# Performance work log

Hardware: AMD Instinct MI355X
Metric: run time of the kernel (lower is better)

The kernel has to match this reference:

```python
import jax, jax.numpy as jnp
import numpy as np

B, T, F, H = 256, 512, 64, 128


def _uniform(key, shape, stdv):
    return jax.random.uniform(key, shape, jnp.float32, -stdv, stdv)


def setup_inputs() -> dict:
    key = jax.random.key(0)
    ks = jax.random.split(key, 24)
    values = jax.random.normal(ks[0], (B, T, F), jnp.float32)
    masks = (jax.random.uniform(ks[1], (B, T, F)) < 0.8).astype(jnp.float32)
    deltas = jax.random.uniform(ks[2], (B, T, F), jnp.float32)
    labels = (jax.random.uniform(ks[3], (B, 1)) < 0.5).astype(jnp.float32)
    is_train = (jax.random.uniform(ks[4], (B, 1)) < 0.8).astype(jnp.float32)
    sH = 1.0 / np.sqrt(H)
    sF = 1.0 / np.sqrt(F)
    # temp_decay_h: Linear F -> H (stdv = 1/sqrt(out) per reset_parameters)
    W_dh = _uniform(ks[5], (H, F), sH); b_dh = _uniform(ks[6], (H,), sH)
    # temp_decay_x: diag F -> F
    W_dx = _uniform(ks[7], (F, F), sF); b_dx = _uniform(ks[8], (F,), sF)
    # hist_reg: Linear H -> F (torch Linear stdv = 1/sqrt(in))
    W_hr = _uniform(ks[9], (F, H), sH); b_hr = _uniform(ks[10], (F,), sH)
    # feat_reg: F -> F with zeroed diagonal mask
    W_fr = _uniform(ks[11], (F, F), sF); b_fr = _uniform(ks[12], (F,), sF)
    # weight_combine: Linear 2F -> F
    s2F = 1.0 / np.sqrt(2 * F)
    W_wc = _uniform(ks[13], (F, 2 * F), s2F); b_wc = _uniform(ks[14], (F,), s2F)
    # LSTMCell(2F, H): torch init uniform(-1/sqrt(H), 1/sqrt(H)), gate order i,f,g,o
    W_ih = _uniform(ks[15], (4 * H, 2 * F), sH); b_ih = _uniform(ks[16], (4 * H,), sH)
    W_hh = _uniform(ks[17], (4 * H, H), sH); b_hh = _uniform(ks[18], (4 * H,), sH)
    # out: Linear H -> 1
    W_out = _uniform(ks[19], (1, H), sH); b_out = _uniform(ks[20], (1,), sH)
    return dict(values=values, masks=masks, deltas=deltas, labels=labels, is_train=is_train,
                W_dh=W_dh, b_dh=b_dh, W_dx=W_dx, b_dx=b_dx, W_hr=W_hr, b_hr=b_hr,
                W_fr=W_fr, b_fr=b_fr, W_wc=W_wc, b_wc=b_wc,
                W_ih=W_ih, b_ih=b_ih, W_hh=W_hh, b_hh=b_hh, W_out=W_out, b_out=b_out)


def _forward(values, masks, deltas, labels, is_train,
             W_dh, b_dh, W_dx, b_dx, W_hr, b_hr, W_fr, b_fr, W_wc, b_wc,
             W_ih, b_ih, W_hh, b_hh, W_out, b_out):
    eps = 1e-5
    w_dx_diag = jnp.diagonal(W_dx)            # diag mask: W * I
    W_fr_m = W_fr * (1.0 - jnp.eye(F, dtype=W_fr.dtype))  # zero diagonal

    def step(carry, xs):
        h, c, x_loss = carry
        x, m, d = xs                           # each [B, F]
        gamma_h = jnp.exp(-jax.nn.relu(d @ W_dh.T + b_dh))   # [B, H]
        gamma_x = jnp.exp(-jax.nn.relu(d * w_dx_diag + b_dx))  # [B, F]
        h = h * gamma_h
        x_h = h @ W_hr.T + b_hr                # [B, F]
        msum = jnp.sum(m) + eps
        x_loss = x_loss + jnp.sum(jnp.abs(x - x_h) * m) / msum
        x_c = m * x + (1.0 - m) * x_h
        z_h = x_c @ W_fr_m.T + b_fr
        x_loss = x_loss + jnp.sum(jnp.abs(x - z_h) * m) / msum
        alpha = jnp.concatenate([gamma_x, m], axis=1) @ W_wc.T + b_wc
        c_h = alpha * z_h + (1.0 - alpha) * x_h
        x_loss = x_loss + jnp.sum(jnp.abs(x - c_h) * m) / msum
        c_c = m * x + (1.0 - m) * c_h
        inp = jnp.concatenate([c_c, m], axis=1)   # [B, 2F]
        gates = inp @ W_ih.T + b_ih + h @ W_hh.T + b_hh  # [B, 4H]
        i, f, g, o = jnp.split(gates, 4, axis=1)
        c = jax.nn.sigmoid(f) * c + jax.nn.sigmoid(i) * jnp.tanh(g)
        h = jax.nn.sigmoid(o) * jnp.tanh(c)
        return (h, c, x_loss), c_c

    h0 = jnp.zeros((values.shape[0], H), values.dtype)
    c0 = jnp.zeros((values.shape[0], H), values.dtype)
    xs = (jnp.swapaxes(values, 0, 1), jnp.swapaxes(masks, 0, 1), jnp.swapaxes(deltas, 0, 1))
    (h, c, x_loss), imps = jax.lax.scan(step, (h0, c0, jnp.float32(0.0)), xs)
    imputations = jnp.swapaxes(imps, 0, 1)     # [B, T, F]
    y_h = h @ W_out.T + b_out                  # [B, 1] logits
    # stable BCE with logits (matches torch reference formula)
    max_val = jnp.maximum(-y_h, 0.0)
    y_l = y_h - y_h * labels + max_val + jnp.log(jnp.exp(-max_val) + jnp.exp(-y_h - max_val))
    y_loss = jnp.sum(y_l * is_train) / (jnp.sum(is_train) + eps)
    loss = x_loss / T + y_loss * 0.3
    predictions = jax.nn.sigmoid(y_h)
    return loss, predictions, imputations


def reference(values, masks, deltas, labels, is_train,
              W_dh, b_dh, W_dx, b_dx, W_hr, b_hr, W_fr, b_fr, W_wc, b_wc,
              W_ih, b_ih, W_hh, b_hh, W_out, b_out):
    return _forward(values, masks, deltas, labels, is_train,
                    W_dh, b_dh, W_dx, b_dx, W_hr, b_hr, W_fr, b_fr, W_wc, b_wc,
                    W_ih, b_ih, W_hh, b_hh, W_out, b_out)
```

## Files before the change

kernel.cpp:

```cpp
#include <hip/hip_runtime.h>
#include <hip/hip_fp16.h>


#define NBATCH 256
#define NT 512
#define NF 64
#define NH 128

#define AFRAG_OFF 0u
#define WHR_OFF   262144u
#define WFR_OFF   278528u
#define INVMS_OFF 286720u
#define ISTR_OFF  288768u
#define GH_OFF    294912u
#define AL_OFF    33849344u

typedef _Float16 half2_t __attribute__((ext_vector_type(2)));
typedef _Float16 half8_t __attribute__((ext_vector_type(8)));
typedef float float4_t __attribute__((ext_vector_type(4)));

__device__ __forceinline__ unsigned pack2(float a, float b) {
    __half2 h = __floats2half2_rn(a, b);
    return __builtin_bit_cast(unsigned, h);
}

__device__ __forceinline__ float dot2f(unsigned w, unsigned a, float acc) {
#if __has_builtin(__builtin_amdgcn_fdot2)
    return __builtin_amdgcn_fdot2(__builtin_bit_cast(half2_t, w),
                                  __builtin_bit_cast(half2_t, a), acc, false);
#else
    float2 wf = __half22float2(__builtin_bit_cast(__half2, w));
    float2 af = __half22float2(__builtin_bit_cast(__half2, a));
    return acc + wf.x * af.x + wf.y * af.y;
#endif
}

__device__ __forceinline__ float4_t mfma16(half8_t a, half8_t b, float4_t c) {
    return __builtin_amdgcn_mfma_f32_16x16x32_f16(a, b, c, 0, 0, 0);
}

__device__ __forceinline__ float sigm(float x) { return 1.f / (1.f + __expf(-x)); }
__device__ __forceinline__ float tanh_fast(float x) { return 1.f - 2.f / (__expf(2.f * x) + 1.f); }

__global__ __launch_bounds__(256) void prep_w(const float* __restrict__ Wih,
                                              const float* __restrict__ Whh,
                                              const float* __restrict__ Whr,
                                              const float* __restrict__ Wfr,
                                              unsigned* __restrict__ wsu) {
    int o = blockIdx.x * 256 + threadIdx.x;
    float v0, v1;
    if (o < 65536) {
        int comp = o & 3;
        int u4 = o >> 2;
        int lane = u4 & 63;
        int tile = u4 >> 6;
        int kt = tile & 7, rt = (tile >> 3) & 3, w = tile >> 5;
        int row = 64 * w + 16 * rt + (lane & 15);
        int kp = 16 * kt + ((lane >> 4) << 2) + comp;
        int k0 = 2 * kp;
        if (k0 < 128) { v0 = Wih[row * 128 + k0]; v1 = Wih[row * 128 + k0 + 1]; }
        else          { v0 = Whh[row * 128 + k0 - 128]; v1 = Whh[row * 128 + k0 - 127]; }
    } else if (o < 69632) {
        int o3 = o - 65536;
        int c = o3 & 3, f = (o3 >> 2) & 63, cb = o3 >> 8;
        int col = 8 * cb + 2 * c;
        v0 = Whr[f * 128 + col]; v1 = Whr[f * 128 + col + 1];
    } else if (o < 71680) {
        int o4 = o - 69632;
        int c = o4 & 3, f = (o4 >> 2) & 63, cb = o4 >> 8;
        int col = 8 * cb + 2 * c;
        v0 = (col == f) ? 0.f : Wfr[f * 64 + col];
        v1 = (col + 1 == f) ? 0.f : Wfr[f * 64 + col + 1];
    } else {
        return;
    }
    wsu[o] = pack2(v0, v1);
}

__global__ __launch_bounds__(256) void prep_msum(const float* __restrict__ masks,
                                                 const float* __restrict__ is_train,
                                                 float* __restrict__ invms,
                                                 float* __restrict__ inv_istr,
                                                 float* __restrict__ d_out0) {
    __shared__ float red[256];
    int tid = threadIdx.x;
    int t = blockIdx.x;
    if (t < NT) {
        int f = tid & 63, br = tid >> 6;
        float s = 0.f;
        for (int i = 0; i < 64; i++) {
            int b = br + i * 4;
            s += masks[((size_t)b * NT + t) * NF + f];
        }
        red[tid] = s;
        __syncthreads();
        for (int off = 128; off > 0; off >>= 1) {
            if (tid < off) red[tid] += red[tid + off];
            __syncthreads();
        }
        if (tid == 0) invms[t] = 1.f / (red[0] + 1e-5f);
    } else {
        red[tid] = is_train[tid];
        __syncthreads();
        for (int off = 128; off > 0; off >>= 1) {
            if (tid < off) red[tid] += red[tid + off];
            __syncthreads();
        }
        if (tid == 0) {
            *inv_istr = 1.f / (red[0] + 1e-5f);
            *d_out0 = 0.f;
        }
    }
}

__global__ __launch_bounds__(256) void ga_kernel(const float* __restrict__ deltas,
                                                 const float* __restrict__ masks,
                                                 const float* __restrict__ Wdh,
                                                 const float* __restrict__ bdh,
                                                 const float* __restrict__ Wdx,
                                                 const float* __restrict__ bdx,
                                                 const float* __restrict__ Wwc,
                                                 const float* __restrict__ bwc,
                                                 __half* __restrict__ gh_all,
                                                 __half* __restrict__ al_all) {
    __shared__ unsigned wdhpk[32 * 128];
    __shared__ unsigned wwcpk[64 * 64];
    __shared__ float sbdh[128], sbdx[64], swdx[64], sbwc[64];
    __shared__ float dbuf[64];
    __shared__ __align__(16) unsigned dpk[32], gxpk[32], mpk2[32];
    int tid = threadIdx.x;

    for (int o = tid; o < 4096; o += 256) {
        int j = o & 127, k2 = o >> 7;
        wdhpk[o] = pack2(Wdh[j * 64 + 2 * k2], Wdh[j * 64 + 2 * k2 + 1]);
    }
    for (int o = tid; o < 4096; o += 256) {
        int f = o & 63, k2 = o >> 6;
        wwcpk[o] = pack2(Wwc[f * 128 + 2 * k2], Wwc[f * 128 + 2 * k2 + 1]);
    }
    if (tid < 128) sbdh[tid] = bdh[tid];
    if (tid < 64) {
        sbdx[tid] = bdx[tid];
        swdx[tid] = Wdx[tid * 65];
        sbwc[tid] = bwc[tid];
    }
    __syncthreads();

    for (int i = 0; i < 8; i++) {
        int p = blockIdx.x * 8 + i;
        if (tid < 32) {
            float2 dv = ((const float2*)(deltas + (size_t)p * NF))[tid];
            dbuf[2 * tid] = dv.x; dbuf[2 * tid + 1] = dv.y;
            dpk[tid] = pack2(dv.x, dv.y);
        } else if (tid < 64) {
            int q = tid - 32;
            float2 mv = ((const float2*)(masks + (size_t)p * NF))[q];
            mpk2[q] = pack2(mv.x, mv.y);
        }
        __syncthreads();
        if (tid < 64) {
            float gx = __expf(-fmaxf(dbuf[tid] * swdx[tid] + sbdx[tid], 0.f));
            float oth = __shfl_xor(gx, 1);
            if (!(tid & 1)) gxpk[tid >> 1] = pack2(gx, oth);
        }
        __syncthreads();
        if (tid < 128) {
            float a0 = sbdh[tid], a1 = 0.f;
            #pragma unroll
            for (int k8 = 0; k8 < 8; k8++) {
                uint4 dp = *(const uint4*)&dpk[4 * k8];
                a0 = dot2f(wdhpk[(4 * k8 + 0) * 128 + tid], dp.x, a0);
                a1 = dot2f(wdhpk[(4 * k8 + 1) * 128 + tid], dp.y, a1);
                a0 = dot2f(wdhpk[(4 * k8 + 2) * 128 + tid], dp.z, a0);
                a1 = dot2f(wdhpk[(4 * k8 + 3) * 128 + tid], dp.w, a1);
            }
            gh_all[(size_t)p * NH + tid] = __float2half(__expf(-fmaxf(a0 + a1, 0.f)));
        } else if (tid < 192) {
            int f = tid - 128;
            float a0 = sbwc[f], a1 = 0.f;
            #pragma unroll
            for (int k8 = 0; k8 < 8; k8++) {
                uint4 gp = *(const uint4*)&gxpk[4 * k8];
                a0 = dot2f(wwcpk[(4 * k8 + 0) * 64 + f], gp.x, a0);
                a1 = dot2f(wwcpk[(4 * k8 + 1) * 64 + f], gp.y, a1);
                a0 = dot2f(wwcpk[(4 * k8 + 2) * 64 + f], gp.z, a0);
                a1 = dot2f(wwcpk[(4 * k8 + 3) * 64 + f], gp.w, a1);
            }
            #pragma unroll
            for (int k8 = 0; k8 < 8; k8++) {
                uint4 mp = *(const uint4*)&mpk2[4 * k8];
                a0 = dot2f(wwcpk[(32 + 4 * k8 + 0) * 64 + f], mp.x, a0);
                a1 = dot2f(wwcpk[(32 + 4 * k8 + 1) * 64 + f], mp.y, a1);
                a0 = dot2f(wwcpk[(32 + 4 * k8 + 2) * 64 + f], mp.z, a0);
                a1 = dot2f(wwcpk[(32 + 4 * k8 + 3) * 64 + f], mp.w, a1);
            }
            al_all[(size_t)p * NF + f] = __float2half(a0 + a1);
        }
        __syncthreads();
    }
}

__global__ __launch_bounds__(512, 2) void main_kernel(
    const float* __restrict__ values, const float* __restrict__ masks,
    const float* __restrict__ labels, const float* __restrict__ is_train,
    const float* __restrict__ b_hr, const float* __restrict__ b_fr,
    const float* __restrict__ b_ih, const float* __restrict__ b_hh,
    const float* __restrict__ W_out, const float* __restrict__ b_out,
    const uint4* __restrict__ afrag_ws, const uint4* __restrict__ whr_ws,
    const uint4* __restrict__ wfr_ws,
    const float* __restrict__ invms, const float* __restrict__ inv_istr,
    const __half* __restrict__ gh_all, const __half* __restrict__ al_all,
    float* __restrict__ d_out) {
    __shared__ __align__(16) uint4 whr4u[16 * 64];
    __shared__ __align__(16) uint4 wfr4u[8 * 64];
    __shared__ float bpart[512], cpart[512], gates[512];
    __shared__ float xbuf[64], mbuf[64], albuf[64];
    __shared__ float sbhr[64], sbfr[64];
    __shared__ __align__(16) unsigned hpk[64];
    __shared__ __align__(16) unsigned mpk[32], xcpk[32], ccpk[32];
    __shared__ float sinv[1];

    const int tid = threadIdx.x;
    const int b = blockIdx.x;
    const int f = tid & 63;
    const int s = tid >> 6;
    const int q4 = (tid >> 4) & 3;

    uint4 afr[4][8];
    #pragma unroll
    for (int rt = 0; rt < 4; rt++)
        #pragma unroll
        for (int kt = 0; kt < 8; kt++) {
            afr[rt][kt] = afrag_ws[(((s * 4 + rt) * 8) + kt) * 64 + f];
            asm volatile("" : "+v"(afr[rt][kt].x), "+v"(afr[rt][kt].y),
                              "+v"(afr[rt][kt].z), "+v"(afr[rt][kt].w));
        }

    float4_t bias_r[4];
    #pragma unroll
    for (int rt = 0; rt < 4; rt++)
        #pragma unroll
        for (int reg = 0; reg < 4; reg++) {
            int row = 64 * s + 16 * rt + 4 * q4 + reg;
            bias_r[rt][reg] = b_ih[row] + b_hh[row];
        }

    for (int o = tid; o < 1024; o += 512) whr4u[o] = whr_ws[o];
    if (tid < 512) wfr4u[tid] = wfr_ws[tid];
    if (tid < 64) { sbhr[tid] = b_hr[tid]; sbfr[tid] = b_fr[tid]; }

    const float* vp = values + (size_t)b * NT * NF;
    const float* mp = masks + (size_t)b * NT * NF;
    const __half* alp = al_all + (size_t)b * NT * NF;
    const __half* ghp = gh_all + (size_t)b * NT * NH;
    float* imp = d_out + 257 + (size_t)b * NT * NF;

    if (tid < 64) {
        float x0 = vp[tid];
        float m0 = mp[tid];
        xbuf[tid] = x0; mbuf[tid] = m0;
        albuf[tid] = __half2float(alp[tid]);
        float m1 = __shfl_xor(m0, 1);
        if (!(tid & 1)) mpk[tid >> 1] = pack2(m0, m1);
        hpk[tid] = 0u;
    }
    if (tid == 64) sinv[0] = invms[0];
    __syncthreads();

    float creg = 0.f, hn = 0.f;
    float lloss = 0.f;

    for (int t = 0; t < NT; t++) {
        int tn = (t + 1 < NT) ? (t + 1) : (NT - 1);
        __half ghn = __float2half(0.f);
        float2 mn2 = make_float2(0.f, 0.f);
        float xn = 0.f, aln = 0.f, invtn = 0.f;
        if (tid < 128) ghn = ghp[(size_t)tn * NH + tid];
        else if (tid < 160) mn2 = ((const float2*)(mp + tn * NF))[tid - 128];
        else if (tid < 256 && tid >= 192) xn = vp[tn * NF + (tid - 192)];
        else if (tid >= 256 && tid < 320) aln = __half2float(alp[tn * NF + (tid - 256)]);
        else if (tid == 320) invtn = invms[tn];

        float4_t acc[4];
        {
            half8_t bh[4];
            #pragma unroll
            for (int j = 0; j < 4; j++)
                bh[j] = *((const half8_t*)&hpk[16 * j + 4 * q4]);
            #pragma unroll
            for (int rt = 0; rt < 4; rt++) {
                acc[rt] = bias_r[rt];
                #pragma unroll
                for (int j = 0; j < 4; j++)
                    acc[rt] = mfma16(__builtin_bit_cast(half8_t, afr[rt][4 + j]), bh[j], acc[rt]);
            }
        }

        {
            uint4 w0 = whr4u[(2 * s) * 64 + f];
            uint4 w1 = whr4u[(2 * s + 1) * 64 + f];
            uint4 h0 = *(const uint4*)&hpk[8 * s];
            uint4 h1 = *(const uint4*)&hpk[8 * s + 4];
            float p0 = 0.f, p1 = 0.f;
            p0 = dot2f(w0.x, h0.x, p0); p1 = dot2f(w0.y, h0.y, p1);
            p0 = dot2f(w0.z, h0.z, p0); p1 = dot2f(w0.w, h0.w, p1);
            p0 = dot2f(w1.x, h1.x, p0); p1 = dot2f(w1.y, h1.y, p1);
            p0 = dot2f(w1.z, h1.z, p0); p1 = dot2f(w1.w, h1.w, p1);
            bpart[s * 64 + f] = p0 + p1;
        }
        __syncthreads();

        float xreg = 0.f, mreg = 0.f, invt = 0.f, xh_keep = 0.f;
        if (tid < 64) {
            float xh = sbhr[f];
            #pragma unroll
            for (int s2 = 0; s2 < 8; s2++) xh += bpart[s2 * 64 + f];
            xreg = xbuf[f]; mreg = mbuf[f]; invt = sinv[0];
            xh_keep = xh;
            float xc = mreg * xreg + (1.f - mreg) * xh;
            lloss += fabsf(xreg - xh) * mreg * invt;
            float oth = __shfl_xor(xc, 1);
            if (!(f & 1)) xcpk[f >> 1] = pack2(xc, oth);
        }
        __syncthreads();

        {
            uint4 w = wfr4u[s * 64 + f];
            uint4 xp = *(const uint4*)&xcpk[4 * s];
            float p0 = 0.f, p1 = 0.f;
            p0 = dot2f(w.x, xp.x, p0); p1 = dot2f(w.y, xp.y, p1);
            p0 = dot2f(w.z, xp.z, p0); p1 = dot2f(w.w, xp.w, p1);
            cpart[s * 64 + f] = p0 + p1;
        }
        __syncthreads();

        if (tid < 64) {
            float zh = sbfr[f];
            #pragma unroll
            for (int s2 = 0; s2 < 8; s2++) zh += cpart[s2 * 64 + f];
            float al = albuf[f];
            float ch = al * zh + (1.f - al) * xh_keep;
            float cc = mreg * xreg + (1.f - mreg) * ch;
            imp[t * NF + f] = cc;
            lloss += (fabsf(xreg - zh) + fabsf(xreg - ch)) * mreg * invt;
            float oth = __shfl_xor(cc, 1);
            if (!(f & 1)) ccpk[f >> 1] = pack2(cc, oth);
        }
        __syncthreads();

        {
            half8_t bc[4];
            bc[0] = *((const half8_t*)&ccpk[4 * q4]);
            bc[1] = *((const half8_t*)&ccpk[16 + 4 * q4]);
            bc[2] = *((const half8_t*)&mpk[4 * q4]);
            bc[3] = *((const half8_t*)&mpk[16 + 4 * q4]);
            #pragma unroll
            for (int rt = 0; rt < 4; rt++) {
                #pragma unroll
                for (int j = 0; j < 4; j++)
                    acc[rt] = mfma16(__builtin_bit_cast(half8_t, afr[rt][j]), bc[j], acc[rt]);
            }
            if ((tid & 15) == 0) {
                #pragma unroll
                for (int rt = 0; rt < 4; rt++)
                    *((float4_t*)&gates[64 * s + 16 * rt + 4 * q4]) = acc[rt];
            }
        }
        __syncthreads();

        if (tid < 128) {
            float gi = gates[tid], gf = gates[128 + tid];
            float gg = gates[256 + tid], go = gates[384 + tid];
            float cn = sigm(gf) * creg + sigm(gi) * tanh_fast(gg);
            creg = cn;
            hn = sigm(go) * tanh_fast(cn);
            float hd = hn * __half2float(ghn);
            float oth = __shfl_xor(hd, 1);
            if (!(tid & 1)) hpk[tid >> 1] = pack2(hd, oth);
        } else if (tid < 160) {
            int q = tid - 128;
            mbuf[2 * q] = mn2.x; mbuf[2 * q + 1] = mn2.y;
            mpk[q] = pack2(mn2.x, mn2.y);
        } else if (tid >= 192 && tid < 256) {
            xbuf[tid - 192] = xn;
        } else if (tid >= 256 && tid < 320) {
            albuf[tid - 256] = aln;
        } else if (tid == 320) {
            sinv[0] = invtn;
        }
        __syncthreads();
    }

    if (tid < 128) bpart[tid] = hn * W_out[tid];
    __syncthreads();
    if (tid < 64) {
        float yp = bpart[tid] + bpart[tid + 64];
        float ll = lloss;
        #pragma unroll
        for (int off = 32; off > 0; off >>= 1) {
            ll += __shfl_down(ll, off);
            yp += __shfl_down(yp, off);
        }
        if (tid == 0) {
            float yh = yp + b_out[0];
            d_out[1 + b] = 1.f / (1.f + expf(-yh));
            float lab = labels[b], istr = is_train[b];
            float maxv = fmaxf(-yh, 0.f);
            float yl = yh - yh * lab + maxv + logf(expf(-maxv) + expf(-yh - maxv));
            atomicAdd(d_out, ll * (1.f / (float)NT) + 0.3f * yl * istr * (*inv_istr));
        }
    }
}

extern "C" void kernel_launch(void* const* d_in, const int* in_sizes, int n_in,
                              void* d_out, int out_size, void* d_ws, size_t ws_size,
                              hipStream_t stream) {
    const float* values = (const float*)d_in[0];
    const float* masks = (const float*)d_in[1];
    const float* deltas = (const float*)d_in[2];
    const float* labels = (const float*)d_in[3];
    const float* is_train = (const float*)d_in[4];
    const float* W_dh = (const float*)d_in[5];
    const float* b_dh = (const float*)d_in[6];
    const float* W_dx = (const float*)d_in[7];
    const float* b_dx = (const float*)d_in[8];
    const float* W_hr = (const float*)d_in[9];
    const float* b_hr = (const float*)d_in[10];
    const float* W_fr = (const float*)d_in[11];
    const float* b_fr = (const float*)d_in[12];
    const float* W_wc = (const float*)d_in[13];
    const float* b_wc = (const float*)d_in[14];
    const float* W_ih = (const float*)d_in[15];
    const float* b_ih = (const float*)d_in[16];
    const float* W_hh = (const float*)d_in[17];
    const float* b_hh = (const float*)d_in[18];
    const float* W_out = (const float*)d_in[19];
    const float* b_out = (const float*)d_in[20];

    char* ws = (char*)d_ws;
    unsigned* wsu = (unsigned*)d_ws;
    const uint4* afrag_ws = (const uint4*)(ws + AFRAG_OFF);
    const uint4* whr_ws = (const uint4*)(ws + WHR_OFF);
    const uint4* wfr_ws = (const uint4*)(ws + WFR_OFF);
    float* invms = (float*)(ws + INVMS_OFF);
    float* inv_istr = (float*)(ws + ISTR_OFF);
    __half* gh_all = (__half*)(ws + GH_OFF);
    __half* al_all = (__half*)(ws + AL_OFF);
    float* out_f = (float*)d_out;

    prep_w<<<280, 256, 0, stream>>>(W_ih, W_hh, W_hr, W_fr, wsu);
    prep_msum<<<513, 256, 0, stream>>>(masks, is_train, invms, inv_istr, out_f);
    ga_kernel<<<16384, 256, 0, stream>>>(deltas, masks, W_dh, b_dh, W_dx, b_dx,
                                         W_wc, b_wc, gh_all, al_all);
    main_kernel<<<NBATCH, 512, 0, stream>>>(values, masks, labels, is_train,
                                            b_hr, b_fr, b_ih, b_hh, W_out, b_out,
                                            afrag_ws, whr_ws, wfr_ws,
                                            invms, inv_istr, gh_all, al_all, out_f);
}
```

Before: 1.509 ms.

## Restructure recurrent main loop, gate-interleaved weights, split mask-sum reduction

The main kernel's timestep loop is reorganised. The W_ih/W_hh fragment layout is permuted so each wave holds all four gates for its hidden rows, which lets the LSTM cell update run straight from MFMA accumulators with no shared-memory gates buffer. The hist_reg and feat_reg dot products now run entirely in wave 0, which cuts per-step barriers from five to two. The mask-sum prep becomes a coalesced two-stage reduction, and ga_kernel handles 64 positions per block instead of 8. The cost is serialising the small matvecs onto one wave and reusing the gh workspace for the partial sums.

```diff
diff --git a/kernel.cpp b/kernel.cpp
--- a/kernel.cpp
+++ b/kernel.cpp
@@ -41,6 +41,8 @@
 
 __device__ __forceinline__ float sigm(float x) { return 1.f / (1.f + __expf(-x)); }
 __device__ __forceinline__ float tanh_fast(float x) { return 1.f - 2.f / (__expf(2.f * x) + 1.f); }
+
+#define PIN4(u) asm volatile("" : "+v"((u).x), "+v"((u).y), "+v"((u).z), "+v"((u).w))
 
 __global__ __launch_bounds__(256) void prep_w(const float* __restrict__ Wih,
                                               const float* __restrict__ Whh,
@@ -54,9 +56,9 @@
         int u4 = o >> 2;
         int lane = u4 & 63;
         int tile = u4 >> 6;
-        int kt = tile & 7, rt = (tile >> 3) & 3, w = tile >> 5;
-        int row = 64 * w + 16 * rt + (lane & 15);
-        int kp = 16 * kt + ((lane >> 4) << 2) + comp;
+        int c = tile & 7, g = (tile >> 3) & 3, s = tile >> 5;
+        int row = 128 * g + 16 * s + (lane & 15);
+        int kp = 16 * c + ((lane >> 4) << 2) + comp;
         int k0 = 2 * kp;
         if (k0 < 128) { v0 = Wih[row * 128 + k0]; v1 = Wih[row * 128 + k0 + 1]; }
         else          { v0 = Whh[row * 128 + k0 - 128]; v1 = Whh[row * 128 + k0 - 127]; }
@@ -77,28 +79,27 @@
     wsu[o] = pack2(v0, v1);
 }
 
-__global__ __launch_bounds__(256) void prep_msum(const float* __restrict__ masks,
-                                                 const float* __restrict__ is_train,
-                                                 float* __restrict__ invms,
-                                                 float* __restrict__ inv_istr,
-                                                 float* __restrict__ d_out0) {
+__global__ __launch_bounds__(256) void prep_msum_part(const float* __restrict__ masks,
+                                                      const float* __restrict__ is_train,
+                                                      float* __restrict__ part,
+                                                      float* __restrict__ d_out0) {
     __shared__ float red[256];
     int tid = threadIdx.x;
-    int t = blockIdx.x;
-    if (t < NT) {
-        int f = tid & 63, br = tid >> 6;
+    int blk = blockIdx.x;
+    if (blk < 4096) {
+        int t = blk >> 3, bc = blk & 7;
+        int r = tid >> 3, fo = (tid & 7) * 8;
+        const float* p = masks + ((size_t)(32 * bc + r) * NT + t) * NF + fo;
         float s = 0.f;
-        for (int i = 0; i < 64; i++) {
-            int b = br + i * 4;
-            s += masks[((size_t)b * NT + t) * NF + f];
-        }
+        #pragma unroll
+        for (int i = 0; i < 8; i++) s += p[i];
         red[tid] = s;
         __syncthreads();
         for (int off = 128; off > 0; off >>= 1) {
             if (tid < off) red[tid] += red[tid + off];
             __syncthreads();
         }
-        if (tid == 0) invms[t] = 1.f / (red[0] + 1e-5f);
+        if (tid == 0) part[blk] = red[0];
     } else {
         red[tid] = is_train[tid];
         __syncthreads();
@@ -106,11 +107,19 @@
             if (tid < off) red[tid] += red[tid + off];
             __syncthreads();
         }
-        if (tid == 0) {
-            *inv_istr = 1.f / (red[0] + 1e-5f);
-            *d_out0 = 0.f;
-        }
-    }
+        if (tid == 0) { part[4096] = red[0]; *d_out0 = 0.f; }
+    }
+}
+
+__global__ __launch_bounds__(512) void finalize_msum(const float* __restrict__ part,
+                                                     float* __restrict__ invms,
+                                                     float* __restrict__ inv_istr) {
+    int tid = threadIdx.x;
+    float s = 0.f;
+    #pragma unroll
+    for (int i = 0; i < 8; i++) s += part[tid * 8 + i];
+    invms[tid] = 1.f / (s + 1e-5f);
+    if (tid == 0) *inv_istr = 1.f / (part[4096] + 1e-5f);
 }
 
 __global__ __launch_bounds__(256) void ga_kernel(const float* __restrict__ deltas,
@@ -146,8 +155,8 @@
     }
     __syncthreads();
 
-    for (int i = 0; i < 8; i++) {
-        int p = blockIdx.x * 8 + i;
+    for (int i = 0; i < 64; i++) {
+        int p = blockIdx.x * 64 + i;
         if (tid < 32) {
             float2 dv = ((const float2*)(deltas + (size_t)p * NF))[tid];
             dbuf[2 * tid] = dv.x; dbuf[2 * tid + 1] = dv.y;
@@ -211,43 +220,40 @@
     const float* __restrict__ invms, const float* __restrict__ inv_istr,
     const __half* __restrict__ gh_all, const __half* __restrict__ al_all,
     float* __restrict__ d_out) {
-    __shared__ __align__(16) uint4 whr4u[16 * 64];
-    __shared__ __align__(16) uint4 wfr4u[8 * 64];
-    __shared__ float bpart[512], cpart[512], gates[512];
-    __shared__ float xbuf[64], mbuf[64], albuf[64];
-    __shared__ float sbhr[64], sbfr[64];
+    __shared__ __align__(16) uint4 whr4u[1024];
+    __shared__ __align__(16) uint4 wfr4u[512];
     __shared__ __align__(16) unsigned hpk[64];
-    __shared__ __align__(16) unsigned mpk[32], xcpk[32], ccpk[32];
-    __shared__ float sinv[1];
+    __shared__ __align__(16) unsigned ccm[64];
+    __shared__ __align__(16) unsigned xcpk[32];
+    __shared__ float hraw[128];
+    __shared__ float rbuf[128];
 
     const int tid = threadIdx.x;
     const int b = blockIdx.x;
-    const int f = tid & 63;
+    const int lane = tid & 63;
     const int s = tid >> 6;
-    const int q4 = (tid >> 4) & 3;
+    const int q = lane >> 4;
+    const int l15 = lane & 15;
 
     uint4 afr[4][8];
     #pragma unroll
-    for (int rt = 0; rt < 4; rt++)
+    for (int g = 0; g < 4; g++)
         #pragma unroll
-        for (int kt = 0; kt < 8; kt++) {
-            afr[rt][kt] = afrag_ws[(((s * 4 + rt) * 8) + kt) * 64 + f];
-            asm volatile("" : "+v"(afr[rt][kt].x), "+v"(afr[rt][kt].y),
-                              "+v"(afr[rt][kt].z), "+v"(afr[rt][kt].w));
-        }
+        for (int c = 0; c < 8; c++)
+            afr[g][c] = afrag_ws[(((s * 4 + g) * 8) + c) * 64 + lane];
 
     float4_t bias_r[4];
     #pragma unroll
-    for (int rt = 0; rt < 4; rt++)
+    for (int g = 0; g < 4; g++)
         #pragma unroll
         for (int reg = 0; reg < 4; reg++) {
-            int row = 64 * s + 16 * rt + 4 * q4 + reg;
-            bias_r[rt][reg] = b_ih[row] + b_hh[row];
+            int row = 128 * g + 16 * s + 4 * q + reg;
+            bias_r[g][reg] = b_ih[row] + b_hh[row];
         }
 
     for (int o = tid; o < 1024; o += 512) whr4u[o] = whr_ws[o];
     if (tid < 512) wfr4u[tid] = wfr_ws[tid];
-    if (tid < 64) { sbhr[tid] = b_hr[tid]; sbfr[tid] = b_fr[tid]; }
+    if (tid < 64) hpk[tid] = 0u;
 
     const float* vp = values + (size_t)b * NT * NF;
     const float* mp = masks + (size_t)b * NT * NF;
@@ -255,146 +261,121 @@
     const __half* ghp = gh_all + (size_t)b * NT * NH;
     float* imp = d_out + 257 + (size_t)b * NT * NF;
 
-    if (tid < 64) {
-        float x0 = vp[tid];
-        float m0 = mp[tid];
-        xbuf[tid] = x0; mbuf[tid] = m0;
-        albuf[tid] = __half2float(alp[tid]);
-        float m1 = __shfl_xor(m0, 1);
-        if (!(tid & 1)) mpk[tid >> 1] = pack2(m0, m1);
-        hpk[tid] = 0u;
-    }
-    if (tid == 64) sinv[0] = invms[0];
+    float cst[4] = {0.f, 0.f, 0.f, 0.f};
+    float lloss = 0.f;
+    float bhr_r = 0.f, bfr_r = 0.f;
+    float xr = 0.f, mr = 0.f, alr = 0.f, invr = 0.f;
+    if (s == 0) {
+        bhr_r = b_hr[lane]; bfr_r = b_fr[lane];
+        xr = vp[lane]; mr = mp[lane];
+        alr = __half2float(alp[lane]); invr = invms[0];
+    }
     __syncthreads();
 
-    float creg = 0.f, hn = 0.f;
-    float lloss = 0.f;
-
     for (int t = 0; t < NT; t++) {
+        #pragma unroll
+        for (int g = 0; g < 4; g++)
+            #pragma unroll
+            for (int c = 0; c < 8; c++)
+                PIN4(afr[g][c]);
+
         int tn = (t + 1 < NT) ? (t + 1) : (NT - 1);
-        __half ghn = __float2half(0.f);
-        float2 mn2 = make_float2(0.f, 0.f);
-        float xn = 0.f, aln = 0.f, invtn = 0.f;
-        if (tid < 128) ghn = ghp[(size_t)tn * NH + tid];
-        else if (tid < 160) mn2 = ((const float2*)(mp + tn * NF))[tid - 128];
-        else if (tid < 256 && tid >= 192) xn = vp[tn * NF + (tid - 192)];
-        else if (tid >= 256 && tid < 320) aln = __half2float(alp[tn * NF + (tid - 256)]);
-        else if (tid == 320) invtn = invms[tn];
+        uint2 ghn = *(const uint2*)(ghp + (size_t)tn * NH + 16 * s + 4 * q);
 
         float4_t acc[4];
         {
             half8_t bh[4];
             #pragma unroll
-            for (int j = 0; j < 4; j++)
-                bh[j] = *((const half8_t*)&hpk[16 * j + 4 * q4]);
-            #pragma unroll
-            for (int rt = 0; rt < 4; rt++) {
-                acc[rt] = bias_r[rt];
+            for (int c2 = 0; c2 < 4; c2++)
+                bh[c2] = *((const half8_t*)&hpk[16 * c2 + 4 * q]);
+            #pragma unroll
+            for (int g = 0; g < 4; g++) {
+                acc[g] = bias_r[g];
                 #pragma unroll
-                for (int j = 0; j < 4; j++)
-                    acc[rt] = mfma16(__builtin_bit_cast(half8_t, afr[rt][4 + j]), bh[j], acc[rt]);
-            }
+                for (int c2 = 0; c2 < 4; c2++)
+                    acc[g] = mfma16(__builtin_bit_cast(half8_t, afr[g][4 + c2]), bh[c2], acc[g]);
+            }
+        }
+
+        if (s == 0) {
+            float a0 = bhr_r, a1 = 0.f, a2 = 0.f, a3 = 0.f;
+            #pragma unroll
+            for (int k4 = 0; k4 < 16; k4++) {
+                uint4 w = whr4u[k4 * 64 + lane];
+                uint4 hp = *(const uint4*)&hpk[4 * k4];
+                a0 = dot2f(w.x, hp.x, a0); a1 = dot2f(w.y, hp.y, a1);
+                a2 = dot2f(w.z, hp.z, a2); a3 = dot2f(w.w, hp.w, a3);
+            }
+            float xh = (a0 + a1) + (a2 + a3);
+            float xc = mr * xr + (1.f - mr) * xh;
+            float oth = __shfl_xor(xc, 1);
+            if (!(lane & 1)) xcpk[lane >> 1] = pack2(xc, oth);
+            float othm = __shfl_xor(mr, 1);
+            if (!(lane & 1)) ccm[32 + (lane >> 1)] = pack2(mr, othm);
+            asm volatile("s_waitcnt lgkmcnt(0)" ::: "memory");
+
+            float c0 = bfr_r, c1 = 0.f, c2 = 0.f, c3 = 0.f;
+            #pragma unroll
+            for (int k4 = 0; k4 < 8; k4++) {
+                uint4 w = wfr4u[k4 * 64 + lane];
+                uint4 xp = *(const uint4*)&xcpk[4 * k4];
+                c0 = dot2f(w.x, xp.x, c0); c1 = dot2f(w.y, xp.y, c1);
+                c2 = dot2f(w.z, xp.z, c2); c3 = dot2f(w.w, xp.w, c3);
+            }
+            float zh = (c0 + c1) + (c2 + c3);
+            float ch = alr * zh + (1.f - alr) * xh;
+            float cc = mr * xr + (1.f - mr) * ch;
+            imp[t * NF + lane] = cc;
+            lloss += (fabsf(xr - xh) + fabsf(xr - zh) + fabsf(xr - ch)) * mr * invr;
+            float othc = __shfl_xor(cc, 1);
+            if (!(lane & 1)) ccm[lane >> 1] = pack2(cc, othc);
+        }
+        __syncthreads();
+
+        if (s == 0) {
+            xr = vp[tn * NF + lane]; mr = mp[tn * NF + lane];
+            alr = __half2float(alp[tn * NF + lane]); invr = invms[tn];
         }
 
         {
-            uint4 w0 = whr4u[(2 * s) * 64 + f];
-            uint4 w1 = whr4u[(2 * s + 1) * 64 + f];
-            uint4 h0 = *(const uint4*)&hpk[8 * s];
-            uint4 h1 = *(const uint4*)&hpk[8 * s + 4];
-            float p0 = 0.f, p1 = 0.f;
-            p0 = dot2f(w0.x, h0.x, p0); p1 = dot2f(w0.y, h0.y, p1);
-            p0 = dot2f(w0.z, h0.z, p0); p1 = dot2f(w0.w, h0.w, p1);
-            p0 = dot2f(w1.x, h1.x, p0); p1 = dot2f(w1.y, h1.y, p1);
-            p0 = dot2f(w1.z, h1.z, p0); p1 = dot2f(w1.w, h1.w, p1);
-            bpart[s * 64 + f] = p0 + p1;
-        }
-        __syncthreads();
-
-        float xreg = 0.f, mreg = 0.f, invt = 0.f, xh_keep = 0.f;
-        if (tid < 64) {
-            float xh = sbhr[f];
-            #pragma unroll
-            for (int s2 = 0; s2 < 8; s2++) xh += bpart[s2 * 64 + f];
-            xreg = xbuf[f]; mreg = mbuf[f]; invt = sinv[0];
-            xh_keep = xh;
-            float xc = mreg * xreg + (1.f - mreg) * xh;
-            lloss += fabsf(xreg - xh) * mreg * invt;
-            float oth = __shfl_xor(xc, 1);
-            if (!(f & 1)) xcpk[f >> 1] = pack2(xc, oth);
-        }
-        __syncthreads();
+            half8_t bc2[4];
+            #pragma unroll
+            for (int c2 = 0; c2 < 4; c2++)
+                bc2[c2] = *((const half8_t*)&ccm[16 * c2 + 4 * q]);
+            #pragma unroll
+            for (int g = 0; g < 4; g++) {
+                #pragma unroll
+                for (int c2 = 0; c2 < 4; c2++)
+                    acc[g] = mfma16(__builtin_bit_cast(half8_t, afr[g][c2]), bc2[c2], acc[g]);
+            }
+        }
 
         {
-            uint4 w = wfr4u[s * 64 + f];
-            uint4 xp = *(const uint4*)&xcpk[4 * s];
-            float p0 = 0.f, p1 = 0.f;
-            p0 = dot2f(w.x, xp.x, p0); p1 = dot2f(w.y, xp.y, p1);
-            p0 = dot2f(w.z, xp.z, p0); p1 = dot2f(w.w, xp.w, p1);
-            cpart[s * 64 + f] = p0 + p1;
-        }
-        __syncthreads();
-
-        if (tid < 64) {
-            float zh = sbfr[f];
-            #pragma unroll
-            for (int s2 = 0; s2 < 8; s2++) zh += cpart[s2 * 64 + f];
-            float al = albuf[f];
-            float ch = al * zh + (1.f - al) * xh_keep;
-            float cc = mreg * xreg + (1.f - mreg) * ch;
-            imp[t * NF + f] = cc;
-            lloss += (fabsf(xreg - zh) + fabsf(xreg - ch)) * mreg * invt;
-            float oth = __shfl_xor(cc, 1);
-            if (!(f & 1)) ccpk[f >> 1] = pack2(cc, oth);
-        }
-        __syncthreads();
-
-        {
-            half8_t bc[4];
-            bc[0] = *((const half8_t*)&ccpk[4 * q4]);
-            bc[1] = *((const half8_t*)&ccpk[16 + 4 * q4]);
-            bc[2] = *((const half8_t*)&mpk[4 * q4]);
-            bc[3] = *((const half8_t*)&mpk[16 + 4 * q4]);
-            #pragma unroll
-            for (int rt = 0; rt < 4; rt++) {
-                #pragma unroll
-                for (int j = 0; j < 4; j++)
-                    acc[rt] = mfma16(__builtin_bit_cast(half8_t, afr[rt][j]), bc[j], acc[rt]);
-            }
-            if ((tid & 15) == 0) {
-                #pragma unroll
-                for (int rt = 0; rt < 4; rt++)
-                    *((float4_t*)&gates[64 * s + 16 * rt + 4 * q4]) = acc[rt];
-            }
-        }
-        __syncthreads();
-
-        if (tid < 128) {
-            float gi = gates[tid], gf = gates[128 + tid];
-            float gg = gates[256 + tid], go = gates[384 + tid];
-            float cn = sigm(gf) * creg + sigm(gi) * tanh_fast(gg);
-            creg = cn;
-            hn = sigm(go) * tanh_fast(cn);
-            float hd = hn * __half2float(ghn);
-            float oth = __shfl_xor(hd, 1);
-            if (!(tid & 1)) hpk[tid >> 1] = pack2(hd, oth);
-        } else if (tid < 160) {
-            int q = tid - 128;
-            mbuf[2 * q] = mn2.x; mbuf[2 * q + 1] = mn2.y;
-            mpk[q] = pack2(mn2.x, mn2.y);
-        } else if (tid >= 192 && tid < 256) {
-            xbuf[tid - 192] = xn;
-        } else if (tid >= 256 && tid < 320) {
-            albuf[tid - 256] = aln;
-        } else if (tid == 320) {
-            sinv[0] = invtn;
-        }
-        __syncthreads();
-    }
-
-    if (tid < 128) bpart[tid] = hn * W_out[tid];
+            float2 g01 = __half22float2(__builtin_bit_cast(__half2, ghn.x));
+            float2 g23 = __half22float2(__builtin_bit_cast(__half2, ghn.y));
+            float hv[4];
+            #pragma unroll
+            for (int reg = 0; reg < 4; reg++) {
+                float gi = acc[0][reg], gf = acc[1][reg];
+                float gg = acc[2][reg], go = acc[3][reg];
+                float cn = sigm(gf) * cst[reg] + sigm(gi) * tanh_fast(gg);
+                cst[reg] = cn;
+                hv[reg] = sigm(go) * tanh_fast(cn);
+            }
+            if (l15 == 0) {
+                *(float4*)&hraw[16 * s + 4 * q] =
+                    make_float4(hv[0], hv[1], hv[2], hv[3]);
+                hpk[8 * s + 2 * q] = pack2(hv[0] * g01.x, hv[1] * g01.y);
+                hpk[8 * s + 2 * q + 1] = pack2(hv[2] * g23.x, hv[3] * g23.y);
+            }
+        }
+        __syncthreads();
+    }
+
+    if (tid < 128) rbuf[tid] = hraw[tid] * W_out[tid];
     __syncthreads();
     if (tid < 64) {
-        float yp = bpart[tid] + bpart[tid + 64];
+        float yp = rbuf[tid] + rbuf[tid + 64];
         float ll = lloss;
         #pragma unroll
         for (int off = 32; off > 0; off >>= 1) {
@@ -444,14 +425,16 @@
     const uint4* wfr_ws = (const uint4*)(ws + WFR_OFF);
     float* invms = (float*)(ws + INVMS_OFF);
     float* inv_istr = (float*)(ws + ISTR_OFF);
+    float* part = (float*)(ws + GH_OFF);
     __half* gh_all = (__half*)(ws + GH_OFF);
     __half* al_all = (__half*)(ws + AL_OFF);
     float* out_f = (float*)d_out;
 
     prep_w<<<280, 256, 0, stream>>>(W_ih, W_hh, W_hr, W_fr, wsu);
-    prep_msum<<<513, 256, 0, stream>>>(masks, is_train, invms, inv_istr, out_f);
-    ga_kernel<<<16384, 256, 0, stream>>>(deltas, masks, W_dh, b_dh, W_dx, b_dx,
-                                         W_wc, b_wc, gh_all, al_all);
+    prep_msum_part<<<4097, 256, 0, stream>>>(masks, is_train, part, out_f);
+    finalize_msum<<<1, 512, 0, stream>>>(part, invms, inv_istr);
+    ga_kernel<<<2048, 256, 0, stream>>>(deltas, masks, W_dh, b_dh, W_dx, b_dx,
+                                        W_wc, b_wc, gh_all, al_all);
     main_kernel<<<NBATCH, 512, 0, stream>>>(values, masks, labels, is_train,
                                             b_hr, b_fr, b_ih, b_hh, W_out, b_out,
                                             afrag_ws, whr_ws, wfr_ws,
```

Result: slower. 2.334 ms (+54.6%).
